# Optimization experiments

Hardware: AMD Instinct MI355X
Metric: run time of the kernel (lower is better)

Reference implementation:

```python
import jax, jax.numpy as jnp
import numpy as np

NUM_EXPERTS = 8
TOP_K = 2
FFN_DIM = 2048   # model dim (input/output of the block)
HIDDEN_DIM = 4096  # expert intermediate dim


def setup_inputs() -> dict:
    key = jax.random.key(0)
    k0, k1, k2, k3, k4 = jax.random.split(key, 5)
    scale = 0.02
    return {
        "hidden_states": jax.random.normal(k0, (2, 1024, FFN_DIM), dtype=jnp.float32),
        "gate_w": jax.random.normal(k1, (NUM_EXPERTS, FFN_DIM), dtype=jnp.float32) * scale,
        "w1": jax.random.normal(k2, (NUM_EXPERTS, FFN_DIM, HIDDEN_DIM), dtype=jnp.float32) * scale,
        "w2": jax.random.normal(k3, (NUM_EXPERTS, HIDDEN_DIM, FFN_DIM), dtype=jnp.float32) * scale,
        "w3": jax.random.normal(k4, (NUM_EXPERTS, FFN_DIM, HIDDEN_DIM), dtype=jnp.float32) * scale,
    }


def reference(hidden_states, gate_w, w1, w2, w3):
    origin_shape = hidden_states.shape
    x = hidden_states.reshape(-1, FFN_DIM)            # [N, F]
    n_tokens = x.shape[0]

    # Router: softmax in fp32, top-k, renormalize, cast back.
    router_logits = x @ gate_w.T                      # [N, E]
    routing_probs = jax.nn.softmax(router_logits.astype(jnp.float32), axis=-1)
    topk_w, topk_idx = jax.lax.top_k(routing_probs, TOP_K)   # [N, K]
    topk_w = topk_w / jnp.sum(topk_w, axis=-1, keepdims=True)
    topk_w = topk_w.astype(x.dtype)

    # Dense per-(token, expert) combine weight; 0 where expert not selected.
    token_ids = jnp.arange(n_tokens)[:, None]         # [N, 1]
    full_w = jnp.zeros((n_tokens, NUM_EXPERTS), dtype=x.dtype)
    full_w = full_w.at[token_ids, topk_idx].add(topk_w)  # [N, E]

    # SiLU-gated MLP per expert (computed densely, masked by full_w).
    h = jax.nn.silu(jnp.einsum("nf,efh->enh", x, w1)) * jnp.einsum("nf,efh->enh", x, w3)
    y = jnp.einsum("enh,ehf->enf", h, w2)             # [E, N, F]
    out = jnp.einsum("enf,ne->nf", y, full_w)         # [N, F]

    return out.reshape(origin_shape)
```

## Files before the change

kernel.cpp:

```cpp
#include <hip/hip_runtime.h>
#include <math.h>

#define NTOK 2048
#define FDIM 2048
#define HDIM 4096
#define NEXP 8
#define MAXPAIR (NTOK * 2)

typedef _Float16 f16;
typedef _Float16 f16x4 __attribute__((ext_vector_type(4)));
typedef _Float16 f16x8 __attribute__((ext_vector_type(8)));
typedef float    f32x4 __attribute__((ext_vector_type(4)));

static constexpr size_t OFF_XH   = 0;
static constexpr size_t OFF_H    = OFF_XH + (size_t)NTOK * FDIM * 2;
static constexpr size_t OFF_Y    = OFF_H + (size_t)(MAXPAIR + 128) * HDIM * 2;
static constexpr size_t OFF_ET   = OFF_Y + (size_t)MAXPAIR * FDIM * 4;
static constexpr size_t OFF_CNT  = OFF_ET + (size_t)NEXP * NTOK * 4;
static constexpr size_t OFF_BASE = OFF_CNT + 128;
static constexpr size_t OFF_TE   = OFF_BASE + 128;
static constexpr size_t OFF_TP   = OFF_TE + (size_t)NTOK * 2 * 4;
static constexpr size_t OFF_TW   = OFF_TP + (size_t)NTOK * 2 * 4;

__global__ __launch_bounds__(256) void convert_zero_kernel(
    const float* __restrict__ x, f16* __restrict__ xh, int* __restrict__ counts)
{
    int i = blockIdx.x * 256 + threadIdx.x;
    float4 v = ((const float4*)x)[i];
    f16x4 h = { (f16)v.x, (f16)v.y, (f16)v.z, (f16)v.w };
    ((f16x4*)xh)[i] = h;
    if (i < NEXP) counts[i] = 0;
}

__global__ __launch_bounds__(64) void router_kernel(
    const float* __restrict__ x, const float* __restrict__ gw,
    int* __restrict__ counts, int* __restrict__ expert_tokens,
    int* __restrict__ tok_e, int* __restrict__ tok_pos, float* __restrict__ tok_w)
{
    const int t = blockIdx.x;
    const int l = threadIdx.x;
    const float* xr = x + (size_t)t * FDIM;
    float xv[FDIM / 64];
    #pragma unroll
    for (int i = 0; i < FDIM / 64; ++i) xv[i] = xr[i * 64 + l];

    float lg[NEXP];
    #pragma unroll
    for (int e = 0; e < NEXP; ++e) {
        const float* g = gw + (size_t)e * FDIM;
        float p = 0.f;
        #pragma unroll
        for (int i = 0; i < FDIM / 64; ++i) p = fmaf(xv[i], g[i * 64 + l], p);
        #pragma unroll
        for (int o = 32; o; o >>= 1) p += __shfl_xor(p, o);
        lg[e] = p;
    }
    if (l == 0) {
        float mx = lg[0];
        #pragma unroll
        for (int e = 1; e < NEXP; ++e) mx = fmaxf(mx, lg[e]);
        float pr[NEXP];
        #pragma unroll
        for (int e = 0; e < NEXP; ++e) pr[e] = expf(lg[e] - mx);
        int i0 = 0;
        #pragma unroll
        for (int e = 1; e < NEXP; ++e) if (pr[e] > pr[i0]) i0 = e;
        int i1 = (i0 == 0) ? 1 : 0;
        #pragma unroll
        for (int e = 0; e < NEXP; ++e) if (e != i0 && pr[e] > pr[i1]) i1 = e;
        float s = pr[i0] + pr[i1];
        float w0 = pr[i0] / s, w1 = pr[i1] / s;
        int p0 = atomicAdd(&counts[i0], 1);
        int p1 = atomicAdd(&counts[i1], 1);
        expert_tokens[i0 * NTOK + p0] = t;
        expert_tokens[i1 * NTOK + p1] = t;
        tok_e[2 * t] = i0;  tok_e[2 * t + 1] = i1;
        tok_pos[2 * t] = p0; tok_pos[2 * t + 1] = p1;
        tok_w[2 * t] = w0;  tok_w[2 * t + 1] = w1;
    }
}

__global__ void bases_kernel(const int* __restrict__ counts, int* __restrict__ bases)
{
    if (threadIdx.x == 0 && blockIdx.x == 0) {
        int s = 0;
        for (int e = 0; e < NEXP; ++e) { bases[e] = s; s += counts[e]; }
    }
}

__global__ __launch_bounds__(256) void gemm1_kernel(
    const f16* __restrict__ xh, const float* __restrict__ w1, const float* __restrict__ w3,
    const int* __restrict__ counts, const int* __restrict__ bases,
    const int* __restrict__ expert_tokens, f16* __restrict__ hbuf)
{
    const int e = blockIdx.x >> 4;
    const int mtile = blockIdx.x & 15;
    const int ntile = blockIdx.y;
    const int cnt = counts[e];
    const int m0 = mtile * 128;
    if (m0 >= cnt) return;
    const int rows = min(128, cnt - m0);
    const int base = bases[e];

    __shared__ f16 As[128 * 32];
    __shared__ f16 Bs1[128 * 36];
    __shared__ f16 Bs3[128 * 36];

    const int tid = threadIdx.x;
    const int lane = tid & 63;
    const int wave = tid >> 6;
    const int wm = wave >> 1, wn = wave & 1;

    const f16* arow[2];
    #pragma unroll
    for (int q = 0; q < 2; ++q) {
        int chunk = q * 256 + tid;
        int row = chunk >> 2, kp = chunk & 3;
        int r = min(row, rows - 1);
        int token = expert_tokens[e * NTOK + m0 + r];
        arow[q] = xh + (size_t)token * FDIM + kp * 8;
    }
    const int n4 = tid & 31, kq = tid >> 5;
    const int n0 = n4 * 4;
    const float* b1p = w1 + (size_t)e * FDIM * HDIM + (size_t)(kq * 4) * HDIM + ntile * 128 + n0;
    const float* b3p = w3 + (size_t)e * FDIM * HDIM + (size_t)(kq * 4) * HDIM + ntile * 128 + n0;

    f32x4 acc1[4][4], acc3[4][4];
    #pragma unroll
    for (int i = 0; i < 4; ++i)
        #pragma unroll
        for (int j = 0; j < 4; ++j) {
            acc1[i][j] = (f32x4){0.f, 0.f, 0.f, 0.f};
            acc3[i][j] = (f32x4){0.f, 0.f, 0.f, 0.f};
        }

    for (int k0 = 0; k0 < FDIM; k0 += 32) {
        uint4 av[2];
        #pragma unroll
        for (int q = 0; q < 2; ++q) av[q] = *(const uint4*)(arow[q] + k0);
        float4 r1[4], r3[4];
        #pragma unroll
        for (int kk = 0; kk < 4; ++kk) {
            r1[kk] = *(const float4*)(b1p + (size_t)(k0 + kk) * HDIM);
            r3[kk] = *(const float4*)(b3p + (size_t)(k0 + kk) * HDIM);
        }
        __syncthreads();
        #pragma unroll
        for (int q = 0; q < 2; ++q)
            *(uint4*)&As[(q * 256 + tid) * 8] = av[q];
        #pragma unroll
        for (int i = 0; i < 4; ++i) {
            f16x4 v1 = { (f16)((const float*)&r1[0])[i], (f16)((const float*)&r1[1])[i],
                         (f16)((const float*)&r1[2])[i], (f16)((const float*)&r1[3])[i] };
            f16x4 v3 = { (f16)((const float*)&r3[0])[i], (f16)((const float*)&r3[1])[i],
                         (f16)((const float*)&r3[2])[i], (f16)((const float*)&r3[3])[i] };
            *(f16x4*)&Bs1[(n0 + i) * 36 + kq * 4] = v1;
            *(f16x4*)&Bs3[(n0 + i) * 36 + kq * 4] = v3;
        }
        __syncthreads();

        f16x8 af[4];
        #pragma unroll
        for (int i = 0; i < 4; ++i)
            af[i] = *(const f16x8*)&As[(wm * 64 + i * 16 + (lane & 15)) * 32 + (lane >> 4) * 8];
        #pragma unroll
        for (int j = 0; j < 4; ++j) {
            const int nn = (wn * 64 + j * 16 + (lane & 15)) * 36 + (lane >> 4) * 8;
            f16x4 b1a = *(const f16x4*)&Bs1[nn];
            f16x4 b1b = *(const f16x4*)&Bs1[nn + 4];
            f16x8 bf1 = __builtin_shufflevector(b1a, b1b, 0, 1, 2, 3, 4, 5, 6, 7);
            f16x4 b3a = *(const f16x4*)&Bs3[nn];
            f16x4 b3b = *(const f16x4*)&Bs3[nn + 4];
            f16x8 bf3 = __builtin_shufflevector(b3a, b3b, 0, 1, 2, 3, 4, 5, 6, 7);
            #pragma unroll
            for (int i = 0; i < 4; ++i) {
                acc1[i][j] = __builtin_amdgcn_mfma_f32_16x16x32_f16(af[i], bf1, acc1[i][j], 0, 0, 0);
                acc3[i][j] = __builtin_amdgcn_mfma_f32_16x16x32_f16(af[i], bf3, acc3[i][j], 0, 0, 0);
            }
        }
    }

    #pragma unroll
    for (int i = 0; i < 4; ++i) {
        int rl0 = wm * 64 + i * 16 + ((lane >> 4) << 2);
        #pragma unroll
        for (int r = 0; r < 4; ++r) {
            int rl = rl0 + r;
            if (rl < rows) {
                size_t ro = (size_t)(base + m0 + rl) * HDIM + ntile * 128 + wn * 64 + (lane & 15);
                #pragma unroll
                for (int j = 0; j < 4; ++j) {
                    float a1 = acc1[i][j][r];
                    float a3 = acc3[i][j][r];
                    float hv = (a1 / (1.f + expf(-a1))) * a3;
                    hbuf[ro + j * 16] = (f16)hv;
                }
            }
        }
    }
}

__global__ __launch_bounds__(256) void gemm2_kernel(
    const f16* __restrict__ hbuf, const float* __restrict__ w2,
    const int* __restrict__ counts, const int* __restrict__ bases,
    float* __restrict__ ybuf)
{
    const int e = blockIdx.x >> 4;
    const int mtile = blockIdx.x & 15;
    const int ntile = blockIdx.y;
    const int cnt = counts[e];
    const int m0 = mtile * 128;
    if (m0 >= cnt) return;
    const int rows = min(128, cnt - m0);
    const int base = bases[e];

    __shared__ f16 As[128 * 32];
    __shared__ f16 Bs[128 * 36];

    const int tid = threadIdx.x;
    const int lane = tid & 63;
    const int wave = tid >> 6;
    const int wm = wave >> 1, wn = wave & 1;

    const f16* arow[2];
    #pragma unroll
    for (int q = 0; q < 2; ++q) {
        int chunk = q * 256 + tid;
        int row = chunk >> 2, kp = chunk & 3;
        arow[q] = hbuf + (size_t)(base + m0 + row) * HDIM + kp * 8;
    }
    const int n4 = tid & 31, kq = tid >> 5;
    const int n0 = n4 * 4;
    const float* b2p = w2 + (size_t)e * HDIM * FDIM + (size_t)(kq * 4) * FDIM + ntile * 128 + n0;

    f32x4 acc[4][4];
    #pragma unroll
    for (int i = 0; i < 4; ++i)
        #pragma unroll
        for (int j = 0; j < 4; ++j) acc[i][j] = (f32x4){0.f, 0.f, 0.f, 0.f};

    for (int k0 = 0; k0 < HDIM; k0 += 32) {
        uint4 av[2];
        #pragma unroll
        for (int q = 0; q < 2; ++q) av[q] = *(const uint4*)(arow[q] + k0);
        float4 rb[4];
        #pragma unroll
        for (int kk = 0; kk < 4; ++kk)
            rb[kk] = *(const float4*)(b2p + (size_t)(k0 + kk) * FDIM);
        __syncthreads();
        #pragma unroll
        for (int q = 0; q < 2; ++q)
            *(uint4*)&As[(q * 256 + tid) * 8] = av[q];
        #pragma unroll
        for (int i = 0; i < 4; ++i) {
            f16x4 v = { (f16)((const float*)&rb[0])[i], (f16)((const float*)&rb[1])[i],
                        (f16)((const float*)&rb[2])[i], (f16)((const float*)&rb[3])[i] };
            *(f16x4*)&Bs[(n0 + i) * 36 + kq * 4] = v;
        }
        __syncthreads();

        f16x8 af[4];
        #pragma unroll
        for (int i = 0; i < 4; ++i)
            af[i] = *(const f16x8*)&As[(wm * 64 + i * 16 + (lane & 15)) * 32 + (lane >> 4) * 8];
        #pragma unroll
        for (int j = 0; j < 4; ++j) {
            const int nn = (wn * 64 + j * 16 + (lane & 15)) * 36 + (lane >> 4) * 8;
            f16x4 ba = *(const f16x4*)&Bs[nn];
            f16x4 bb = *(const f16x4*)&Bs[nn + 4];
            f16x8 bf = __builtin_shufflevector(ba, bb, 0, 1, 2, 3, 4, 5, 6, 7);
            #pragma unroll
            for (int i = 0; i < 4; ++i)
                acc[i][j] = __builtin_amdgcn_mfma_f32_16x16x32_f16(af[i], bf, acc[i][j], 0, 0, 0);
        }
    }

    #pragma unroll
    for (int i = 0; i < 4; ++i) {
        int rl0 = wm * 64 + i * 16 + ((lane >> 4) << 2);
        #pragma unroll
        for (int r = 0; r < 4; ++r) {
            int rl = rl0 + r;
            if (rl < rows) {
                size_t ro = (size_t)(base + m0 + rl) * FDIM + ntile * 128 + wn * 64 + (lane & 15);
                #pragma unroll
                for (int j = 0; j < 4; ++j)
                    ybuf[ro + j * 16] = acc[i][j][r];
            }
        }
    }
}

__global__ __launch_bounds__(256) void combine_kernel(
    const float* __restrict__ ybuf, const int* __restrict__ tok_e,
    const int* __restrict__ tok_pos, const float* __restrict__ tok_w,
    const int* __restrict__ bases, float* __restrict__ out)
{
    int idx = blockIdx.x * 256 + threadIdx.x;
    int t = idx >> 9;
    int f = (idx & 511) << 2;
    int e0 = tok_e[2 * t], e1 = tok_e[2 * t + 1];
    int s0 = bases[e0] + tok_pos[2 * t];
    int s1 = bases[e1] + tok_pos[2 * t + 1];
    float w0 = tok_w[2 * t], w1 = tok_w[2 * t + 1];
    float4 y0 = *(const float4*)&ybuf[(size_t)s0 * FDIM + f];
    float4 y1 = *(const float4*)&ybuf[(size_t)s1 * FDIM + f];
    float4 o = { w0 * y0.x + w1 * y1.x, w0 * y0.y + w1 * y1.y,
                 w0 * y0.z + w1 * y1.z, w0 * y0.w + w1 * y1.w };
    *(float4*)&out[(size_t)t * FDIM + f] = o;
}

extern "C" void kernel_launch(void* const* d_in, const int* in_sizes, int n_in,
                              void* d_out, int out_size, void* d_ws, size_t ws_size,
                              hipStream_t stream)
{
    const float* x  = (const float*)d_in[0];
    const float* gw = (const float*)d_in[1];
    const float* w1 = (const float*)d_in[2];
    const float* w2 = (const float*)d_in[3];
    const float* w3 = (const float*)d_in[4];
    float* out = (float*)d_out;

    char* ws = (char*)d_ws;
    f16*   xh            = (f16*)(ws + OFF_XH);
    f16*   hbuf          = (f16*)(ws + OFF_H);
    float* ybuf          = (float*)(ws + OFF_Y);
    int*   expert_tokens = (int*)(ws + OFF_ET);
    int*   counts        = (int*)(ws + OFF_CNT);
    int*   bases         = (int*)(ws + OFF_BASE);
    int*   tok_e         = (int*)(ws + OFF_TE);
    int*   tok_pos       = (int*)(ws + OFF_TP);
    float* tok_w         = (float*)(ws + OFF_TW);

    convert_zero_kernel<<<NTOK * FDIM / 4 / 256, 256, 0, stream>>>(x, xh, counts);
    router_kernel<<<NTOK, 64, 0, stream>>>(x, gw, counts, expert_tokens, tok_e, tok_pos, tok_w);
    bases_kernel<<<1, 64, 0, stream>>>(counts, bases);
    gemm1_kernel<<<dim3(NEXP * 16, HDIM / 128), 256, 0, stream>>>(
        xh, w1, w3, counts, bases, expert_tokens, hbuf);
    gemm2_kernel<<<dim3(NEXP * 16, FDIM / 128), 256, 0, stream>>>(
        hbuf, w2, counts, bases, ybuf);
    combine_kernel<<<NTOK * FDIM / 4 / 256, 256, 0, stream>>>(
        ybuf, tok_e, tok_pos, tok_w, bases, out);
}
```

Measured before the change: 3.065 ms.

## Prefetch next K-slab into registers, shrink gemm1 N-tile, regroup grid by expert

Both expert GEMMs now load the next K-slab of activations and weights into registers while MFMAs run on the current shared-memory tile, so global-load latency can overlap compute. gemm1's N tile is halved from 128 to 64 to offset the extra prefetch registers and raise the block count. The grid is reordered so the M and N tiles vary within blockIdx.x and the expert sits in blockIdx.y, which changes which blocks run together and how weights are reused in cache. gemm2 also clamps A-row indices so tail rows never read past the valid range.

```diff
diff --git a/kernel.cpp b/kernel.cpp
--- a/kernel.cpp
+++ b/kernel.cpp
@@ -8,6 +8,7 @@
 #define MAXPAIR (NTOK * 2)
 
 typedef _Float16 f16;
+typedef _Float16 f16x2 __attribute__((ext_vector_type(2)));
 typedef _Float16 f16x4 __attribute__((ext_vector_type(4)));
 typedef _Float16 f16x8 __attribute__((ext_vector_type(8)));
 typedef float    f32x4 __attribute__((ext_vector_type(4)));
@@ -93,9 +94,9 @@
     const int* __restrict__ counts, const int* __restrict__ bases,
     const int* __restrict__ expert_tokens, f16* __restrict__ hbuf)
 {
-    const int e = blockIdx.x >> 4;
     const int mtile = blockIdx.x & 15;
-    const int ntile = blockIdx.y;
+    const int ntile = blockIdx.x >> 4;
+    const int e = blockIdx.y;
     const int cnt = counts[e];
     const int m0 = mtile * 128;
     if (m0 >= cnt) return;
@@ -103,8 +104,8 @@
     const int base = bases[e];
 
     __shared__ f16 As[128 * 32];
-    __shared__ f16 Bs1[128 * 36];
-    __shared__ f16 Bs3[128 * 36];
+    __shared__ f16 Bs1[64 * 36];
+    __shared__ f16 Bs3[64 * 36];
 
     const int tid = threadIdx.x;
     const int lane = tid & 63;
@@ -120,52 +121,62 @@
         int token = expert_tokens[e * NTOK + m0 + r];
         arow[q] = xh + (size_t)token * FDIM + kp * 8;
     }
-    const int n4 = tid & 31, kq = tid >> 5;
+    const int n4 = tid & 15, kq = tid >> 4;
     const int n0 = n4 * 4;
-    const float* b1p = w1 + (size_t)e * FDIM * HDIM + (size_t)(kq * 4) * HDIM + ntile * 128 + n0;
-    const float* b3p = w3 + (size_t)e * FDIM * HDIM + (size_t)(kq * 4) * HDIM + ntile * 128 + n0;
-
-    f32x4 acc1[4][4], acc3[4][4];
+    const float* b1p = w1 + (size_t)e * FDIM * HDIM + (size_t)(kq * 2) * HDIM + ntile * 64 + n0;
+    const float* b3p = w3 + (size_t)e * FDIM * HDIM + (size_t)(kq * 2) * HDIM + ntile * 64 + n0;
+
+    f32x4 acc1[4][2], acc3[4][2];
     #pragma unroll
     for (int i = 0; i < 4; ++i)
         #pragma unroll
-        for (int j = 0; j < 4; ++j) {
+        for (int j = 0; j < 2; ++j) {
             acc1[i][j] = (f32x4){0.f, 0.f, 0.f, 0.f};
             acc3[i][j] = (f32x4){0.f, 0.f, 0.f, 0.f};
         }
 
+    uint4 av[2];
+    float4 r1v[2], r3v[2];
+    #pragma unroll
+    for (int q = 0; q < 2; ++q) av[q] = *(const uint4*)(arow[q]);
+    #pragma unroll
+    for (int kk = 0; kk < 2; ++kk) {
+        r1v[kk] = *(const float4*)(b1p + (size_t)kk * HDIM);
+        r3v[kk] = *(const float4*)(b3p + (size_t)kk * HDIM);
+    }
+
     for (int k0 = 0; k0 < FDIM; k0 += 32) {
-        uint4 av[2];
-        #pragma unroll
-        for (int q = 0; q < 2; ++q) av[q] = *(const uint4*)(arow[q] + k0);
-        float4 r1[4], r3[4];
-        #pragma unroll
-        for (int kk = 0; kk < 4; ++kk) {
-            r1[kk] = *(const float4*)(b1p + (size_t)(k0 + kk) * HDIM);
-            r3[kk] = *(const float4*)(b3p + (size_t)(k0 + kk) * HDIM);
-        }
         __syncthreads();
         #pragma unroll
         for (int q = 0; q < 2; ++q)
             *(uint4*)&As[(q * 256 + tid) * 8] = av[q];
         #pragma unroll
         for (int i = 0; i < 4; ++i) {
-            f16x4 v1 = { (f16)((const float*)&r1[0])[i], (f16)((const float*)&r1[1])[i],
-                         (f16)((const float*)&r1[2])[i], (f16)((const float*)&r1[3])[i] };
-            f16x4 v3 = { (f16)((const float*)&r3[0])[i], (f16)((const float*)&r3[1])[i],
-                         (f16)((const float*)&r3[2])[i], (f16)((const float*)&r3[3])[i] };
-            *(f16x4*)&Bs1[(n0 + i) * 36 + kq * 4] = v1;
-            *(f16x4*)&Bs3[(n0 + i) * 36 + kq * 4] = v3;
+            f16x2 v1 = { (f16)((const float*)&r1v[0])[i], (f16)((const float*)&r1v[1])[i] };
+            f16x2 v3 = { (f16)((const float*)&r3v[0])[i], (f16)((const float*)&r3v[1])[i] };
+            *(f16x2*)&Bs1[(n0 + i) * 36 + kq * 2] = v1;
+            *(f16x2*)&Bs3[(n0 + i) * 36 + kq * 2] = v3;
         }
         __syncthreads();
+
+        if (k0 + 32 < FDIM) {
+            const int kn = k0 + 32;
+            #pragma unroll
+            for (int q = 0; q < 2; ++q) av[q] = *(const uint4*)(arow[q] + kn);
+            #pragma unroll
+            for (int kk = 0; kk < 2; ++kk) {
+                r1v[kk] = *(const float4*)(b1p + (size_t)(kn + kk) * HDIM);
+                r3v[kk] = *(const float4*)(b3p + (size_t)(kn + kk) * HDIM);
+            }
+        }
 
         f16x8 af[4];
         #pragma unroll
         for (int i = 0; i < 4; ++i)
             af[i] = *(const f16x8*)&As[(wm * 64 + i * 16 + (lane & 15)) * 32 + (lane >> 4) * 8];
         #pragma unroll
-        for (int j = 0; j < 4; ++j) {
-            const int nn = (wn * 64 + j * 16 + (lane & 15)) * 36 + (lane >> 4) * 8;
+        for (int j = 0; j < 2; ++j) {
+            const int nn = (wn * 32 + j * 16 + (lane & 15)) * 36 + (lane >> 4) * 8;
             f16x4 b1a = *(const f16x4*)&Bs1[nn];
             f16x4 b1b = *(const f16x4*)&Bs1[nn + 4];
             f16x8 bf1 = __builtin_shufflevector(b1a, b1b, 0, 1, 2, 3, 4, 5, 6, 7);
@@ -187,9 +198,9 @@
         for (int r = 0; r < 4; ++r) {
             int rl = rl0 + r;
             if (rl < rows) {
-                size_t ro = (size_t)(base + m0 + rl) * HDIM + ntile * 128 + wn * 64 + (lane & 15);
+                size_t ro = (size_t)(base + m0 + rl) * HDIM + ntile * 64 + wn * 32 + (lane & 15);
                 #pragma unroll
-                for (int j = 0; j < 4; ++j) {
+                for (int j = 0; j < 2; ++j) {
                     float a1 = acc1[i][j][r];
                     float a3 = acc3[i][j][r];
                     float hv = (a1 / (1.f + expf(-a1))) * a3;
@@ -205,9 +216,9 @@
     const int* __restrict__ counts, const int* __restrict__ bases,
     float* __restrict__ ybuf)
 {
-    const int e = blockIdx.x >> 4;
     const int mtile = blockIdx.x & 15;
-    const int ntile = blockIdx.y;
+    const int ntile = blockIdx.x >> 4;
+    const int e = blockIdx.y;
     const int cnt = counts[e];
     const int m0 = mtile * 128;
     if (m0 >= cnt) return;
@@ -227,7 +238,8 @@
     for (int q = 0; q < 2; ++q) {
         int chunk = q * 256 + tid;
         int row = chunk >> 2, kp = chunk & 3;
-        arow[q] = hbuf + (size_t)(base + m0 + row) * HDIM + kp * 8;
+        int r = min(row, rows - 1);
+        arow[q] = hbuf + (size_t)(base + m0 + r) * HDIM + kp * 8;
     }
     const int n4 = tid & 31, kq = tid >> 5;
     const int n0 = n4 * 4;
@@ -239,14 +251,14 @@
         #pragma unroll
         for (int j = 0; j < 4; ++j) acc[i][j] = (f32x4){0.f, 0.f, 0.f, 0.f};
 
+    uint4 av[2];
+    float4 rb[4];
+    #pragma unroll
+    for (int q = 0; q < 2; ++q) av[q] = *(const uint4*)(arow[q]);
+    #pragma unroll
+    for (int kk = 0; kk < 4; ++kk) rb[kk] = *(const float4*)(b2p + (size_t)kk * FDIM);
+
     for (int k0 = 0; k0 < HDIM; k0 += 32) {
-        uint4 av[2];
-        #pragma unroll
-        for (int q = 0; q < 2; ++q) av[q] = *(const uint4*)(arow[q] + k0);
-        float4 rb[4];
-        #pragma unroll
-        for (int kk = 0; kk < 4; ++kk)
-            rb[kk] = *(const float4*)(b2p + (size_t)(k0 + kk) * FDIM);
         __syncthreads();
         #pragma unroll
         for (int q = 0; q < 2; ++q)
@@ -258,6 +270,15 @@
             *(f16x4*)&Bs[(n0 + i) * 36 + kq * 4] = v;
         }
         __syncthreads();
+
+        if (k0 + 32 < HDIM) {
+            const int kn = k0 + 32;
+            #pragma unroll
+            for (int q = 0; q < 2; ++q) av[q] = *(const uint4*)(arow[q] + kn);
+            #pragma unroll
+            for (int kk = 0; kk < 4; ++kk)
+                rb[kk] = *(const float4*)(b2p + (size_t)(kn + kk) * FDIM);
+        }
 
         f16x8 af[4];
         #pragma unroll
@@ -335,9 +356,9 @@
     convert_zero_kernel<<<NTOK * FDIM / 4 / 256, 256, 0, stream>>>(x, xh, counts);
     router_kernel<<<NTOK, 64, 0, stream>>>(x, gw, counts, expert_tokens, tok_e, tok_pos, tok_w);
     bases_kernel<<<1, 64, 0, stream>>>(counts, bases);
-    gemm1_kernel<<<dim3(NEXP * 16, HDIM / 128), 256, 0, stream>>>(
+    gemm1_kernel<<<dim3(16 * (HDIM / 64), NEXP), 256, 0, stream>>>(
         xh, w1, w3, counts, bases, expert_tokens, hbuf);
-    gemm2_kernel<<<dim3(NEXP * 16, FDIM / 128), 256, 0, stream>>>(
+    gemm2_kernel<<<dim3(16 * (FDIM / 128), NEXP), 256, 0, stream>>>(
         hbuf, w2, counts, bases, ybuf);
     combine_kernel<<<NTOK * FDIM / 4 / 256, 256, 0, stream>>>(
         ybuf, tok_e, tok_pos, tok_w, bases, out);
```

Result: faster. 2.843 ms (-7.2%).
